# Kernel tuning notes

Hardware: AMD Instinct MI355X
Metric: run time of the kernel (lower is better)

## Reference

```python
import jax, jax.numpy as jnp
import numpy as np

EMBED_DIM = 256
NUM_HEADS = 8
HEAD_DIM = 32
INNER = NUM_HEADS * HEAD_DIM
NEG_SLOPE = 0.2


def setup_inputs() -> dict:
    key = jax.random.key(0)
    ks = jax.random.split(key, 8)
    B, Ns, Nt = 8, 1024, 1024
    src = jax.random.normal(ks[0], (B, Ns, EMBED_DIM), dtype=jnp.float32)
    trg = jax.random.normal(ks[1], (B, Nt, EMBED_DIM), dtype=jnp.float32)
    src_mask = jnp.ones((B, Ns), dtype=bool)
    trg_mask = jax.random.randint(ks[2], (B, Nt), 0, 2).astype(bool)
    # learned params (xavier-ish scale)
    def xavier(k, shape):
        fan_in, fan_out = shape[0], shape[-1]
        lim = (6.0 / (fan_in + fan_out)) ** 0.5
        return jax.random.uniform(k, shape, jnp.float32, -lim, lim)
    W_src = xavier(ks[3], (EMBED_DIM, INNER))
    W_trg = xavier(ks[4], (EMBED_DIM, INNER))  # is_cross_type=True -> independent
    a_src = xavier(ks[5], (NUM_HEADS, HEAD_DIM))
    a_trg = xavier(ks[6], (NUM_HEADS, HEAD_DIM))
    W_out = xavier(ks[7], (INNER, EMBED_DIM))
    return {"src": src, "trg": trg, "src_mask": src_mask, "trg_mask": trg_mask,
            "W_src": W_src, "W_trg": W_trg, "a_src": a_src, "a_trg": a_trg, "W_out": W_out}


def reference(src, trg, src_mask, trg_mask, W_src, W_trg, a_src, a_trg, W_out):
    B, Ns, _ = src.shape
    Nt = trg.shape[1]
    NH, Dh = NUM_HEADS, HEAD_DIM
    src_proj = (src @ W_src).reshape(B, Ns, NH, Dh)  # dropout p=0
    trg_proj = (trg @ W_trg).reshape(B, Nt, NH, Dh)
    score_src = jnp.einsum('bshd,hd->bsh', src_proj, a_src)
    score_trg = jnp.einsum('bthd,hd->bth', trg_proj, a_trg)
    # (B,Ns,NH,1) + (B,1,NH,Nt) -> (B,Ns,NH,Nt)
    scores = score_src[:, :, :, None] + jnp.transpose(score_trg, (0, 2, 1))[:, None, :, :]
    scores = jnp.where(scores >= 0, scores, NEG_SLOPE * scores)  # LeakyReLU
    edge_mask = src_mask[:, :, None, None] & trg_mask[:, None, None, :]
    scores = jnp.where(edge_mask, scores, -jnp.inf)
    attn = jax.nn.softmax(scores, axis=-1)
    attn = jnp.nan_to_num(attn, nan=0.0)
    aggregated = jnp.einsum('bsht,bthd->bshd', attn, trg_proj)
    output = aggregated.reshape(B, Ns, NH * Dh) @ W_out
    return output, jnp.transpose(attn, (0, 2, 1, 3))
```

## Files before the change

kernel.cpp:

```cpp
#include <hip/hip_runtime.h>
#include <hip/hip_bf16.h>
#include <math.h>

#define NB 8
#define NS 1024
#define NT 1024
#define NE 256
#define NHEADS 8
#define DH 32
#define LOG2E 1.4426950408889634f

typedef __attribute__((ext_vector_type(8))) short short8;
typedef __attribute__((ext_vector_type(8))) unsigned short ushort8;
typedef __attribute__((ext_vector_type(4))) float f32x4;

#define O_VT    0u
#define O_WTT   (8u<<20)
#define O_WTO   ((8u<<20)+131072u)
#define O_CSRC  ((8u<<20)+262144u)
#define O_CTRG  (O_CSRC+8192u)
#define O_SSRC  (O_CTRG+8192u)
#define O_STRG  (O_SSRC+262144u)
#define O_FLAG  (O_STRG+262144u)
#define O_EST   (12u<<20)
#define O_RF    (13u<<20)

__device__ __forceinline__ unsigned short f2bf(float f) {
    __hip_bfloat16 h = __float2bfloat16(f);
    union { __hip_bfloat16 h; unsigned short u; } c; c.h = h;
    return c.u;
}
__device__ __forceinline__ float leaky(float v) {
    return (v >= 0.f) ? v : 0.2f * v;
}
__device__ __forceinline__ float exp2_fast(float x) {
    float r;
    asm("v_exp_f32 %0, %1" : "=v"(r) : "v"(x));
    return r;
}

__global__ __launch_bounds__(256) void setup_kernel(
    const unsigned* __restrict__ tmask_dw, const float* __restrict__ Wsrc,
    const float* __restrict__ Wtrg, const float* __restrict__ Wout,
    const float* __restrict__ asrc, const float* __restrict__ atrg,
    float* __restrict__ c_src, float* __restrict__ c_trg,
    unsigned short* __restrict__ Wt_t, unsigned short* __restrict__ Wt_o,
    int* __restrict__ flag) {
    __shared__ __align__(16) char sm[16640];
    const int tid = threadIdx.x;
    const int bid = blockIdx.x;

    if (bid == 0) {
        __shared__ int s_ok;
        if (tid == 0) s_ok = 1;
        __syncthreads();
        for (int i = tid; i < 2048; i += 256)
            if (tmask_dw[i] > 1u) s_ok = 0;
        __syncthreads();
        if (tid == 0) *flag = s_ok;
    } else if (bid <= 2) {
        float* a_sh = (float*)sm;
        const float* W = (bid == 1) ? Wsrc : Wtrg;
        const float* a = (bid == 1) ? asrc : atrg;
        float* c = (bid == 1) ? c_src : c_trg;
        a_sh[tid] = a[tid];
        __syncthreads();
        const int e = tid;
        float ch[8];
#pragma unroll
        for (int h = 0; h < 8; ++h) ch[h] = 0.f;
        for (int i = 0; i < 64; ++i) {
            const float4 wv = *(const float4*)&W[(size_t)e * NE + i * 4];
            const int h = i >> 3, d0 = (i & 7) * 4;
            ch[h] += wv.x * a_sh[h * 32 + d0] + wv.y * a_sh[h * 32 + d0 + 1] +
                     wv.z * a_sh[h * 32 + d0 + 2] + wv.w * a_sh[h * 32 + d0 + 3];
        }
#pragma unroll
        for (int h = 0; h < 8; ++h) c[h * NE + e] = ch[h];
    } else {
        const int q = bid - 3;
        const float* W = (q >> 4) ? Wout : Wtrg;
        unsigned short* Wt = (q >> 4) ? Wt_o : Wt_t;
        const int tl = q & 15;
        const int k0 = (tl >> 2) * 64, n0 = (tl & 3) * 64;
        float* xs = (float*)sm;
#pragma unroll
        for (int it = 0; it < 4; ++it) {
            const int slot = it * 256 + tid;
            const int k = slot >> 4, c4 = slot & 15;
            const float4 v = *(const float4*)&W[(size_t)(k0 + k) * NE + n0 + c4 * 4];
            float* p = &xs[k * 65 + c4 * 4];
            p[0] = v.x; p[1] = v.y; p[2] = v.z; p[3] = v.w;
        }
        __syncthreads();
#pragma unroll
        for (int it = 0; it < 2; ++it) {
            const int slot = it * 256 + tid;
            const int n = slot >> 3, kc = slot & 7;
            ushort8 v;
#pragma unroll
            for (int e = 0; e < 8; ++e)
                v[e] = f2bf(xs[(kc * 8 + e) * 65 + n]);
            *(ushort8*)&Wt[(size_t)(n0 + n) * NE + k0 + kc * 8] = v;
        }
    }
}

__global__ __launch_bounds__(256) void mid_kernel(
    const float* __restrict__ src, const float* __restrict__ trg,
    const float* __restrict__ c_src, const float* __restrict__ c_trg,
    const unsigned short* __restrict__ Wt_t, unsigned short* __restrict__ Vt,
    float* __restrict__ ssrc, float* __restrict__ strg,
    const void* __restrict__ tmask, const int* __restrict__ flag_p,
    float2* __restrict__ estg) {
    __shared__ __align__(16) char sm[49152];
    const int tid = threadIdx.x;
    const int bid = blockIdx.x;

    if (bid < 256) {
        unsigned short* As = (unsigned short*)sm;
        unsigned short* ldsT = (unsigned short*)(sm + 32768);
        const int lane = tid & 63, w = tid >> 6;
        const int row0 = (bid >> 1) * 64;
        const int col0 = (bid & 1) * 128;

#pragma unroll
        for (int it = 0; it < 8; ++it) {
            const int gf = it * 256 + tid;
            const int row = gf >> 5, g3 = gf & 31;
            const float4 a = *(const float4*)&trg[(size_t)(row0 + row) * NE + g3 * 8];
            const float4 b = *(const float4*)&trg[(size_t)(row0 + row) * NE + g3 * 8 + 4];
            ushort8 v;
            v[0] = f2bf(a.x); v[1] = f2bf(a.y); v[2] = f2bf(a.z); v[3] = f2bf(a.w);
            v[4] = f2bf(b.x); v[5] = f2bf(b.y); v[6] = f2bf(b.z); v[7] = f2bf(b.w);
            *(ushort8*)&As[row * NE + ((g3 ^ (row & 7)) * 8)] = v;
        }
        __syncthreads();

        const int r = lane & 15, g = lane >> 4;
        short8 af[8];
#pragma unroll
        for (int kk = 0; kk < 8; ++kk)
            af[kk] = *(const short8*)&As[(w * 16 + r) * NE + (((kk * 4 + g) ^ (r & 7)) * 8)];

        f32x4 acc[8];
#pragma unroll
        for (int nt = 0; nt < 8; ++nt) acc[nt] = (f32x4){0.f, 0.f, 0.f, 0.f};
#pragma unroll
        for (int kk = 0; kk < 8; ++kk) {
#pragma unroll
            for (int nt = 0; nt < 8; ++nt) {
                const int col = col0 + nt * 16 + r;
                const short8 bf = *(const short8*)&Wt_t[(size_t)col * NE + kk * 32 + g * 8];
                acc[nt] = __builtin_amdgcn_mfma_f32_16x16x32_bf16(af[kk], bf, acc[nt], 0, 0, 0);
            }
        }
        __syncthreads();

#pragma unroll
        for (int nt = 0; nt < 8; ++nt) {
            const int cl = nt * 16 + r;
            const int sw = (cl & 7) << 3;
#pragma unroll
            for (int j = 0; j < 4; ++j) {
                const int t = w * 16 + g * 4 + j;
                ldsT[cl * 64 + (t ^ sw)] = f2bf(acc[nt][j]);
            }
        }
        __syncthreads();

        const int b = row0 >> 10, t0 = row0 & 1023;
#pragma unroll
        for (int it = 0; it < 4; ++it) {
            const int slot = it * 256 + tid;
            const int cl = slot >> 3, ch = slot & 7;
            const int colg = col0 + cl;
            const int h = colg >> 5, d = colg & 31;
            *(ushort8*)&Vt[(((size_t)(b * 8 + h)) * 32 + d) * 1024 + t0 + ch * 8] =
                *(const ushort8*)&ldsT[cl * 64 + ch * 8];
        }
    } else {
        float* xs = (float*)sm;
        float* cs = (float*)(sm + 32768);
        const int rowg0 = (bid - 256) * 32;
        const bool is_src = rowg0 < NB * NS;
        const float* X = is_src ? (src + (size_t)rowg0 * NE)
                                : (trg + (size_t)(rowg0 - NB * NS) * NE);
        const float* C = is_src ? c_src : c_trg;
        float* S = is_src ? (ssrc + (size_t)rowg0 * NHEADS)
                          : (strg + (size_t)(rowg0 - NB * NS) * NHEADS);

#pragma unroll
        for (int it = 0; it < 8; ++it) {
            const int slot = it * 256 + tid;
            const int row = slot >> 6, c4 = slot & 63;
            *(float4*)&xs[row * NE + c4 * 4] =
                *(const float4*)&X[(size_t)row * NE + c4 * 4];
            cs[slot] = C[slot];
        }
        __syncthreads();

        const int r = tid >> 3, h = tid & 7;
        float s = 0.f;
        for (int e = 0; e < NE; e += 4) {
            const float4 x = *(const float4*)&xs[r * NE + e];
            const float4 c = *(const float4*)&cs[h * NE + e];
            s += x.x * c.x + x.y * c.y + x.z * c.z + x.w * c.w;
        }
        S[(size_t)r * NHEADS + h] = s;

        if (!is_src) {
            const int rowg = rowg0 - NB * NS + r;
            const int flag = *flag_p;
            const bool mv = flag ? (((const int*)tmask)[rowg] != 0)
                                 : (((const unsigned char*)tmask)[rowg] != 0);
            const int bb = rowg >> 10, tt = rowg & 1023;
            const float s2 = s * LOG2E;
            float2 e;
            e.x = mv ? exp2_fast(s2) : 0.f;
            e.y = mv ? exp2_fast(0.2f * s2) : 0.f;
            estg[(size_t)(bb * 8 + h) * 1024 + tt] = e;
        }
    }
}

__global__ __launch_bounds__(512) void aggout_kernel(
    const float* __restrict__ ssrc, const float* __restrict__ strg,
    const void* __restrict__ smask, const void* __restrict__ tmask,
    const int* __restrict__ flag_p, const unsigned short* __restrict__ Vt,
    const unsigned short* __restrict__ Wt_o,
    float4* __restrict__ rfg, float* __restrict__ out) {
    const int blk = blockIdx.x;
    const int q = blk & 63;
    const int b = blk >> 6;
    const int tid = threadIdx.x;
    const int lane = tid & 63;
    const int w = tid >> 6;
    const int flag = *flag_p;

    __shared__ __align__(16) float s_sm[8][1024];
    __shared__ __align__(16) unsigned short agg_sw[16 * 256];
    __shared__ float s_inv[8][16];

    for (int t = tid; t < NT; t += 512) {
        const bool mv = flag ? (((const int*)tmask)[b * NT + t] != 0)
                             : (((const unsigned char*)tmask)[b * NT + t] != 0);
        const float4 s0 = *(const float4*)&strg[((size_t)b * NT + t) * 8];
        const float4 s1 = *(const float4*)&strg[((size_t)b * NT + t) * 8 + 4];
        const float sv[8] = {s0.x, s0.y, s0.z, s0.w, s1.x, s1.y, s1.z, s1.w};
#pragma unroll
        for (int h = 0; h < 8; ++h)
            s_sm[h][t] = mv ? sv[h] * LOG2E : -1e30f;
    }
    __syncthreads();

    const int r = lane & 15;
    const int g = lane >> 4;
    const int srow = q * 16 + r;
    const bool rowv = flag ? (((const int*)smask)[b * NS + srow] != 0)
                           : (((const unsigned char*)smask)[b * NS + srow] != 0);
    const int sw = (r & 7) << 3;
    const int h = w;
    const float ss2 = ssrc[((size_t)b * NS + srow) * NHEADS + h] * LOG2E;
    const unsigned short* vr0 = Vt + (size_t)(b * 8 + h) * 32768 + r * 1024;
    const unsigned short* vr1 = vr0 + 16 * 1024;

    f32x4 acc0 = {0.f, 0.f, 0.f, 0.f};
    f32x4 acc1 = {0.f, 0.f, 0.f, 0.f};
    float sum = 0.f;
#pragma unroll 4
    for (int c = 0; c < 32; ++c) {
        const int tb = c * 32 + g * 8;
        const short8 b0 = *(const short8*)&vr0[tb ^ sw];
        const short8 b1 = *(const short8*)&vr1[tb ^ sw];
        const float4 v0 = *(const float4*)&s_sm[h][tb];
        const float4 v1 = *(const float4*)&s_sm[h][tb + 4];
        const float vv[8] = {v0.x, v0.y, v0.z, v0.w, v1.x, v1.y, v1.z, v1.w};
        short8 pa;
#pragma unroll
        for (int e = 0; e < 8; ++e) {
            const float p = exp2_fast(leaky(ss2 + vv[e]));
            sum += p;
            pa[e] = (short)f2bf(p);
        }
        acc0 = __builtin_amdgcn_mfma_f32_16x16x32_bf16(pa, b0, acc0, 0, 0, 0);
        acc1 = __builtin_amdgcn_mfma_f32_16x16x32_bf16(pa, b1, acc1, 0, 0, 0);
    }
    sum += __shfl_xor(sum, 16);
    sum += __shfl_xor(sum, 32);
    const float inv = (rowv && sum > 0.f) ? 1.f / sum : 0.f;
    if (g == 0) {
        s_inv[h][r] = inv;
        float4 rf;
        rf.x = exp2_fast(ss2) * inv;
        rf.y = exp2_fast(0.2f * ss2) * inv;
        rf.z = exp2_fast(-ss2);
        rf.w = 0.f;
        rfg[(size_t)(b * 8 + h) * 1024 + srow] = rf;
    }
    __syncthreads();

#pragma unroll
    for (int j = 0; j < 4; ++j) {
        const int row = g * 4 + j;
        const float iv = s_inv[h][row];
        int col = h * 32 + r;
        agg_sw[row * 256 + ((((col >> 3) ^ (row & 7)) << 3) | (col & 7))] =
            f2bf(acc0[j] * iv);
        col += 16;
        agg_sw[row * 256 + ((((col >> 3) ^ (row & 7)) << 3) | (col & 7))] =
            f2bf(acc1[j] * iv);
    }
    __syncthreads();

    f32x4 oacc[2];
#pragma unroll
    for (int nt = 0; nt < 2; ++nt) oacc[nt] = (f32x4){0.f, 0.f, 0.f, 0.f};
#pragma unroll
    for (int kk = 0; kk < 8; ++kk) {
        const short8 af = *(const short8*)&agg_sw[r * 256 + (((kk * 4 + g) ^ (r & 7)) * 8)];
#pragma unroll
        for (int nt = 0; nt < 2; ++nt) {
            const int col = w * 32 + nt * 16 + r;
            const short8 bf = *(const short8*)&Wt_o[(size_t)col * NE + kk * 32 + g * 8];
            oacc[nt] = __builtin_amdgcn_mfma_f32_16x16x32_bf16(af, bf, oacc[nt], 0, 0, 0);
        }
    }
#pragma unroll
    for (int nt = 0; nt < 2; ++nt) {
        const int col = w * 32 + nt * 16 + r;
#pragma unroll
        for (int j = 0; j < 4; ++j)
            out[((size_t)b * NS + q * 16 + g * 4 + j) * NE + col] = oacc[nt][j];
    }
}

__global__ __launch_bounds__(256) void attn_kernel(
    const float4* __restrict__ rfg, const float4* __restrict__ est4,
    float* __restrict__ attn) {
    const int blk = blockIdx.x;
    const int sg = blk & 127, bh = blk >> 7;
    const int tid = threadIdx.x;

    const float4 p01 = est4[(size_t)bh * 512 + tid * 2];
    const float4 p23 = est4[(size_t)bh * 512 + tid * 2 + 1];
    const float4* rfb = rfg + (size_t)bh * 1024 + sg * 8;
    float* abase = attn + ((size_t)bh * NS + sg * 8) * NT + tid * 4;

#pragma unroll
    for (int rr = 0; rr < 8; ++rr) {
        const float4 rf = rfb[rr];
        float4 o;
        o.x = (p01.x >= rf.z) ? p01.x * rf.x : p01.y * rf.y;
        o.y = (p01.z >= rf.z) ? p01.z * rf.x : p01.w * rf.y;
        o.z = (p23.x >= rf.z) ? p23.x * rf.x : p23.y * rf.y;
        o.w = (p23.z >= rf.z) ? p23.z * rf.x : p23.w * rf.y;
        *(float4*)&abase[(size_t)rr * NT] = o;
    }
}

extern "C" void kernel_launch(void* const* d_in, const int* in_sizes, int n_in,
                              void* d_out, int out_size, void* d_ws, size_t ws_size,
                              hipStream_t stream) {
    const float* src   = (const float*)d_in[0];
    const float* trg   = (const float*)d_in[1];
    const void*  smask = d_in[2];
    const void*  tmask = d_in[3];
    const float* Wsrc  = (const float*)d_in[4];
    const float* Wtrg  = (const float*)d_in[5];
    const float* asrc  = (const float*)d_in[6];
    const float* atrg  = (const float*)d_in[7];
    const float* Wout  = (const float*)d_in[8];

    float* out  = (float*)d_out;
    float* attn = out + (size_t)NB * NS * NE;

    char* wsb = (char*)d_ws;
    unsigned short* Vt   = (unsigned short*)(wsb + O_VT);
    unsigned short* Wt_t = (unsigned short*)(wsb + O_WTT);
    unsigned short* Wt_o = (unsigned short*)(wsb + O_WTO);
    float* c_src = (float*)(wsb + O_CSRC);
    float* c_trg = (float*)(wsb + O_CTRG);
    float* ssrc  = (float*)(wsb + O_SSRC);
    float* strg  = (float*)(wsb + O_STRG);
    int*   flag  = (int*)(wsb + O_FLAG);
    float2* estg = (float2*)(wsb + O_EST);
    float4* rfg  = (float4*)(wsb + O_RF);

    setup_kernel<<<35, 256, 0, stream>>>(
        (const unsigned*)tmask, Wsrc, Wtrg, Wout, asrc, atrg,
        c_src, c_trg, Wt_t, Wt_o, flag);

    mid_kernel<<<768, 256, 0, stream>>>(
        src, trg, c_src, c_trg, Wt_t, Vt, ssrc, strg, tmask, flag, estg);

    aggout_kernel<<<NB * (NS / 16), 512, 0, stream>>>(
        ssrc, strg, smask, tmask, flag, Vt, Wt_o, rfg, out);

    attn_kernel<<<64 * 128, 256, 0, stream>>>(
        rfg, (const float4*)estg, attn);
}
```

Baseline: 107.0 us.

## Merge aggregation and attention-write kernels into one interleaved launch

```diff
diff --git a/kernel.cpp b/kernel.cpp
--- a/kernel.cpp
+++ b/kernel.cpp
@@ -23,7 +23,6 @@
 #define O_STRG  (O_SSRC+262144u)
 #define O_FLAG  (O_STRG+262144u)
 #define O_EST   (12u<<20)
-#define O_RF    (13u<<20)
 
 __device__ __forceinline__ unsigned short f2bf(float f) {
     __hip_bfloat16 h = __float2bfloat16(f);
@@ -224,138 +223,159 @@
     }
 }
 
-__global__ __launch_bounds__(512) void aggout_kernel(
+__global__ __launch_bounds__(512) void combo_kernel(
     const float* __restrict__ ssrc, const float* __restrict__ strg,
     const void* __restrict__ smask, const void* __restrict__ tmask,
     const int* __restrict__ flag_p, const unsigned short* __restrict__ Vt,
-    const unsigned short* __restrict__ Wt_o,
-    float4* __restrict__ rfg, float* __restrict__ out) {
-    const int blk = blockIdx.x;
-    const int q = blk & 63;
-    const int b = blk >> 6;
+    const unsigned short* __restrict__ Wt_o, const float2* __restrict__ estg,
+    float* __restrict__ attn, float* __restrict__ out) {
+    __shared__ __align__(16) char sm[41472];
+    const int bid = blockIdx.x;
     const int tid = threadIdx.x;
     const int lane = tid & 63;
     const int w = tid >> 6;
     const int flag = *flag_p;
 
-    __shared__ __align__(16) float s_sm[8][1024];
-    __shared__ __align__(16) unsigned short agg_sw[16 * 256];
-    __shared__ float s_inv[8][16];
-
-    for (int t = tid; t < NT; t += 512) {
-        const bool mv = flag ? (((const int*)tmask)[b * NT + t] != 0)
-                             : (((const unsigned char*)tmask)[b * NT + t] != 0);
-        const float4 s0 = *(const float4*)&strg[((size_t)b * NT + t) * 8];
-        const float4 s1 = *(const float4*)&strg[((size_t)b * NT + t) * 8 + 4];
-        const float sv[8] = {s0.x, s0.y, s0.z, s0.w, s1.x, s1.y, s1.z, s1.w};
-#pragma unroll
-        for (int h = 0; h < 8; ++h)
-            s_sm[h][t] = mv ? sv[h] * LOG2E : -1e30f;
-    }
-    __syncthreads();
-
-    const int r = lane & 15;
-    const int g = lane >> 4;
-    const int srow = q * 16 + r;
-    const bool rowv = flag ? (((const int*)smask)[b * NS + srow] != 0)
-                           : (((const unsigned char*)smask)[b * NS + srow] != 0);
-    const int sw = (r & 7) << 3;
-    const int h = w;
-    const float ss2 = ssrc[((size_t)b * NS + srow) * NHEADS + h] * LOG2E;
-    const unsigned short* vr0 = Vt + (size_t)(b * 8 + h) * 32768 + r * 1024;
-    const unsigned short* vr1 = vr0 + 16 * 1024;
-
-    f32x4 acc0 = {0.f, 0.f, 0.f, 0.f};
-    f32x4 acc1 = {0.f, 0.f, 0.f, 0.f};
-    float sum = 0.f;
+    if ((bid & 1) == 0) {
+        const int idx = bid >> 1;
+        const int q = idx & 63;
+        const int b = idx >> 6;
+        float* s_sm = (float*)sm;
+        unsigned short* agg_sw = (unsigned short*)(sm + 32768);
+        float* s_inv = (float*)(sm + 32768 + 8192);
+
+        for (int t = tid; t < NT; t += 512) {
+            const bool mv = flag ? (((const int*)tmask)[b * NT + t] != 0)
+                                 : (((const unsigned char*)tmask)[b * NT + t] != 0);
+            const float4 s0 = *(const float4*)&strg[((size_t)b * NT + t) * 8];
+            const float4 s1 = *(const float4*)&strg[((size_t)b * NT + t) * 8 + 4];
+            const float sv[8] = {s0.x, s0.y, s0.z, s0.w, s1.x, s1.y, s1.z, s1.w};
+#pragma unroll
+            for (int h = 0; h < 8; ++h)
+                s_sm[h * 1024 + t] = mv ? sv[h] * LOG2E : -1e30f;
+        }
+        __syncthreads();
+
+        const int r = lane & 15;
+        const int g = lane >> 4;
+        const int srow = q * 16 + r;
+        const bool rowv = flag ? (((const int*)smask)[b * NS + srow] != 0)
+                               : (((const unsigned char*)smask)[b * NS + srow] != 0);
+        const int sw = (r & 7) << 3;
+        const int h = w;
+        const float ss2 = ssrc[((size_t)b * NS + srow) * NHEADS + h] * LOG2E;
+        const unsigned short* vr0 = Vt + (size_t)(b * 8 + h) * 32768 + r * 1024;
+        const unsigned short* vr1 = vr0 + 16 * 1024;
+
+        f32x4 acc0 = {0.f, 0.f, 0.f, 0.f};
+        f32x4 acc1 = {0.f, 0.f, 0.f, 0.f};
+        float sum = 0.f;
 #pragma unroll 4
-    for (int c = 0; c < 32; ++c) {
-        const int tb = c * 32 + g * 8;
-        const short8 b0 = *(const short8*)&vr0[tb ^ sw];
-        const short8 b1 = *(const short8*)&vr1[tb ^ sw];
-        const float4 v0 = *(const float4*)&s_sm[h][tb];
-        const float4 v1 = *(const float4*)&s_sm[h][tb + 4];
-        const float vv[8] = {v0.x, v0.y, v0.z, v0.w, v1.x, v1.y, v1.z, v1.w};
-        short8 pa;
-#pragma unroll
-        for (int e = 0; e < 8; ++e) {
-            const float p = exp2_fast(leaky(ss2 + vv[e]));
-            sum += p;
-            pa[e] = (short)f2bf(p);
-        }
-        acc0 = __builtin_amdgcn_mfma_f32_16x16x32_bf16(pa, b0, acc0, 0, 0, 0);
-        acc1 = __builtin_amdgcn_mfma_f32_16x16x32_bf16(pa, b1, acc1, 0, 0, 0);
-    }
-    sum += __shfl_xor(sum, 16);
-    sum += __shfl_xor(sum, 32);
-    const float inv = (rowv && sum > 0.f) ? 1.f / sum : 0.f;
-    if (g == 0) {
-        s_inv[h][r] = inv;
-        float4 rf;
-        rf.x = exp2_fast(ss2) * inv;
-        rf.y = exp2_fast(0.2f * ss2) * inv;
-        rf.z = exp2_fast(-ss2);
-        rf.w = 0.f;
-        rfg[(size_t)(b * 8 + h) * 1024 + srow] = rf;
-    }
-    __syncthreads();
-
-#pragma unroll
-    for (int j = 0; j < 4; ++j) {
-        const int row = g * 4 + j;
-        const float iv = s_inv[h][row];
-        int col = h * 32 + r;
-        agg_sw[row * 256 + ((((col >> 3) ^ (row & 7)) << 3) | (col & 7))] =
-            f2bf(acc0[j] * iv);
-        col += 16;
-        agg_sw[row * 256 + ((((col >> 3) ^ (row & 7)) << 3) | (col & 7))] =
-            f2bf(acc1[j] * iv);
-    }
-    __syncthreads();
-
-    f32x4 oacc[2];
-#pragma unroll
-    for (int nt = 0; nt < 2; ++nt) oacc[nt] = (f32x4){0.f, 0.f, 0.f, 0.f};
-#pragma unroll
-    for (int kk = 0; kk < 8; ++kk) {
-        const short8 af = *(const short8*)&agg_sw[r * 256 + (((kk * 4 + g) ^ (r & 7)) * 8)];
+        for (int c = 0; c < 32; ++c) {
+            const int tb = c * 32 + g * 8;
+            const short8 b0 = *(const short8*)&vr0[tb ^ sw];
+            const short8 b1 = *(const short8*)&vr1[tb ^ sw];
+            const float4 v0 = *(const float4*)&s_sm[h * 1024 + tb];
+            const float4 v1 = *(const float4*)&s_sm[h * 1024 + tb + 4];
+            const float vv[8] = {v0.x, v0.y, v0.z, v0.w, v1.x, v1.y, v1.z, v1.w};
+            short8 pa;
+#pragma unroll
+            for (int e = 0; e < 8; ++e) {
+                const float p = exp2_fast(leaky(ss2 + vv[e]));
+                sum += p;
+                pa[e] = (short)f2bf(p);
+            }
+            acc0 = __builtin_amdgcn_mfma_f32_16x16x32_bf16(pa, b0, acc0, 0, 0, 0);
+            acc1 = __builtin_amdgcn_mfma_f32_16x16x32_bf16(pa, b1, acc1, 0, 0, 0);
+        }
+        sum += __shfl_xor(sum, 16);
+        sum += __shfl_xor(sum, 32);
+        const float inv = (rowv && sum > 0.f) ? 1.f / sum : 0.f;
+        if (g == 0) s_inv[h * 16 + r] = inv;
+        __syncthreads();
+
+#pragma unroll
+        for (int j = 0; j < 4; ++j) {
+            const int row = g * 4 + j;
+            const float iv = s_inv[h * 16 + row];
+            int col = h * 32 + r;
+            agg_sw[row * 256 + ((((col >> 3) ^ (row & 7)) << 3) | (col & 7))] =
+                f2bf(acc0[j] * iv);
+            col += 16;
+            agg_sw[row * 256 + ((((col >> 3) ^ (row & 7)) << 3) | (col & 7))] =
+                f2bf(acc1[j] * iv);
+        }
+        __syncthreads();
+
+        f32x4 oacc[2];
+#pragma unroll
+        for (int nt = 0; nt < 2; ++nt) oacc[nt] = (f32x4){0.f, 0.f, 0.f, 0.f};
+#pragma unroll
+        for (int kk = 0; kk < 8; ++kk) {
+            const short8 af = *(const short8*)&agg_sw[r * 256 + (((kk * 4 + g) ^ (r & 7)) * 8)];
+#pragma unroll
+            for (int nt = 0; nt < 2; ++nt) {
+                const int col = w * 32 + nt * 16 + r;
+                const short8 bf = *(const short8*)&Wt_o[(size_t)col * NE + kk * 32 + g * 8];
+                oacc[nt] = __builtin_amdgcn_mfma_f32_16x16x32_bf16(af, bf, oacc[nt], 0, 0, 0);
+            }
+        }
 #pragma unroll
         for (int nt = 0; nt < 2; ++nt) {
             const int col = w * 32 + nt * 16 + r;
-            const short8 bf = *(const short8*)&Wt_o[(size_t)col * NE + kk * 32 + g * 8];
-            oacc[nt] = __builtin_amdgcn_mfma_f32_16x16x32_bf16(af, bf, oacc[nt], 0, 0, 0);
-        }
-    }
-#pragma unroll
-    for (int nt = 0; nt < 2; ++nt) {
-        const int col = w * 32 + nt * 16 + r;
-#pragma unroll
-        for (int j = 0; j < 4; ++j)
-            out[((size_t)b * NS + q * 16 + g * 4 + j) * NE + col] = oacc[nt][j];
-    }
-}
-
-__global__ __launch_bounds__(256) void attn_kernel(
-    const float4* __restrict__ rfg, const float4* __restrict__ est4,
-    float* __restrict__ attn) {
-    const int blk = blockIdx.x;
-    const int sg = blk & 127, bh = blk >> 7;
-    const int tid = threadIdx.x;
-
-    const float4 p01 = est4[(size_t)bh * 512 + tid * 2];
-    const float4 p23 = est4[(size_t)bh * 512 + tid * 2 + 1];
-    const float4* rfb = rfg + (size_t)bh * 1024 + sg * 8;
-    float* abase = attn + ((size_t)bh * NS + sg * 8) * NT + tid * 4;
-
-#pragma unroll
-    for (int rr = 0; rr < 8; ++rr) {
-        const float4 rf = rfb[rr];
-        float4 o;
-        o.x = (p01.x >= rf.z) ? p01.x * rf.x : p01.y * rf.y;
-        o.y = (p01.z >= rf.z) ? p01.z * rf.x : p01.w * rf.y;
-        o.z = (p23.x >= rf.z) ? p23.x * rf.x : p23.y * rf.y;
-        o.w = (p23.z >= rf.z) ? p23.z * rf.x : p23.w * rf.y;
-        *(float4*)&abase[(size_t)rr * NT] = o;
+#pragma unroll
+            for (int j = 0; j < 4; ++j)
+                out[((size_t)b * NS + q * 16 + g * 4 + j) * NE + col] = oacc[nt][j];
+        }
+    } else {
+        const int idx = bid >> 1;
+        const int b = idx >> 6;
+        const int h = (idx >> 3) & 7;
+        const int hq = idx & 7;
+
+        float2 e[16];
+        const float2* eb = estg + (size_t)(b * 8 + h) * 1024;
+#pragma unroll
+        for (int qq = 0; qq < 4; ++qq) {
+            const float4 p0 = *(const float4*)&eb[qq * 256 + lane * 4];
+            const float4 p1 = *(const float4*)&eb[qq * 256 + lane * 4 + 2];
+            e[qq * 4 + 0] = make_float2(p0.x, p0.y);
+            e[qq * 4 + 1] = make_float2(p0.z, p0.w);
+            e[qq * 4 + 2] = make_float2(p1.x, p1.y);
+            e[qq * 4 + 3] = make_float2(p1.z, p1.w);
+        }
+
+        const int row0 = hq * 128 + w * 16;
+        for (int rr = 0; rr < 16; ++rr) {
+            const int srow = row0 + rr;
+            const float ss2 = ssrc[((size_t)b * NS + srow) * NHEADS + h] * LOG2E;
+            const bool rowv = flag ? (((const int*)smask)[b * NS + srow] != 0)
+                                   : (((const unsigned char*)smask)[b * NS + srow] != 0);
+            const float e1 = exp2_fast(ss2);
+            const float e2 = exp2_fast(0.2f * ss2);
+            const float thr = exp2_fast(-ss2);
+
+            float sum = 0.f;
+#pragma unroll
+            for (int k = 0; k < 16; ++k)
+                sum += (e[k].x >= thr) ? e[k].x * e1 : e[k].y * e2;
+#pragma unroll
+            for (int off = 32; off >= 1; off >>= 1)
+                sum += __shfl_xor(sum, off);
+            const float inv = (rowv && sum > 0.f) ? 1.f / sum : 0.f;
+            const float v1 = e1 * inv, v2 = e2 * inv;
+
+            float* arow = attn + ((size_t)(b * NHEADS + h) * NS + srow) * NT;
+#pragma unroll
+            for (int qq = 0; qq < 4; ++qq) {
+                float4 o;
+                o.x = (e[qq * 4 + 0].x >= thr) ? e[qq * 4 + 0].x * v1 : e[qq * 4 + 0].y * v2;
+                o.y = (e[qq * 4 + 1].x >= thr) ? e[qq * 4 + 1].x * v1 : e[qq * 4 + 1].y * v2;
+                o.z = (e[qq * 4 + 2].x >= thr) ? e[qq * 4 + 2].x * v1 : e[qq * 4 + 2].y * v2;
+                o.w = (e[qq * 4 + 3].x >= thr) ? e[qq * 4 + 3].x * v1 : e[qq * 4 + 3].y * v2;
+                *(float4*)&arow[qq * 256 + lane * 4] = o;
+            }
+        }
     }
 }
 
@@ -385,7 +405,6 @@
     float* strg  = (float*)(wsb + O_STRG);
     int*   flag  = (int*)(wsb + O_FLAG);
     float2* estg = (float2*)(wsb + O_EST);
-    float4* rfg  = (float4*)(wsb + O_RF);
 
     setup_kernel<<<35, 256, 0, stream>>>(
         (const unsigned*)tmask, Wsrc, Wtrg, Wout, asrc, atrg,
@@ -394,9 +413,6 @@
     mid_kernel<<<768, 256, 0, stream>>>(
         src, trg, c_src, c_trg, Wt_t, Vt, ssrc, strg, tmask, flag, estg);
 
-    aggout_kernel<<<NB * (NS / 16), 512, 0, stream>>>(
-        ssrc, strg, smask, tmask, flag, Vt, Wt_o, rfg, out);
-
-    attn_kernel<<<64 * 128, 256, 0, stream>>>(
-        rfg, (const float4*)estg, attn);
-}
+    combo_kernel<<<1024, 512, 0, stream>>>(
+        ssrc, strg, smask, tmask, flag, Vt, Wt_o, estg, attn, out);
+}
```

Result: faster. 94.37 us (-11.8%).
